# Kernel optimization log

Hardware: AMD Instinct MI355X
Metric: run time of the kernel (lower is better)

Reference implementation:

```python
import jax, jax.numpy as jnp
import numpy as np


def _next_pow2(n: int) -> int:
    return 1 << (int(n) - 1).bit_length()


def setup_inputs() -> dict:
    key = jax.random.key(0)
    k1, k2 = jax.random.split(key)
    B, T, L = 256, 65536, 65536  # batch, seq_len, filter length (L >= T so epoched recurrence == full causal conv)
    x = jax.random.normal(k1, (B, T), dtype=jnp.float32)
    filt = jax.random.normal(k2, (1, L), dtype=jnp.float32) / np.float32(np.sqrt(L))
    return {"x": x, "filt": filt}


def reference(x, filt):
    """EpochedFutureFill.forward == causal FIR convolution of x with filt.

    The torch module's per-token loop (sliced dot-product + FFT-refreshed
    FutureFill cache every K steps) computes exactly
        y[:, t] = sum_{s=0}^{t} filt[0, s] * x[:, t - s]
    for t < T <= L. We express that directly as one FFT convolution,
    mirroring the module's own future_fill (pow-2 rfft/irfft) math.
    """
    B, T = x.shape
    L = filt.shape[-1]
    n_fft = _next_pow2(T + L - 1)
    xf = jnp.fft.rfft(x, n=n_fft)        # (B, n_fft//2+1) complex
    ff = jnp.fft.rfft(filt, n=n_fft)     # (1, n_fft//2+1) complex, broadcasts over batch
    y_full = jnp.fft.irfft(xf * ff, n=n_fft)
    return y_full[:, :T]                 # causal part: (B, T)
```

## Files before the change

kernel.cpp:

```cpp
#include <hip/hip_runtime.h>


#define N_FFT 131072
#define N1    512
#define N2    256
#define T_LEN 65536
#define CB    128
#define PI_F  3.14159265358979323846f
#define R2_F  0.70710678118654752f
#define C16F  0.92387953251128675613f
#define S16F  0.38268343236508977173f

typedef __attribute__((ext_vector_type(2))) __fp16 h2;
typedef __attribute__((ext_vector_type(4))) __fp16 h4;
typedef __attribute__((ext_vector_type(8))) __fp16 h8;

__device__ inline int brev9(int x) { return (int)(__brev((unsigned)x) >> 23); }

__device__ inline float2 cadd(float2 a, float2 b){ return make_float2(a.x+b.x, a.y+b.y); }
__device__ inline float2 csub(float2 a, float2 b){ return make_float2(a.x-b.x, a.y-b.y); }
__device__ inline float2 cmul(float2 a, float2 b){ return make_float2(a.x*b.x-a.y*b.y, a.x*b.y+a.y*b.x); }
__device__ inline float2 cmulc(float2 a, float2 b){ return make_float2(a.x*b.x+a.y*b.y, a.y*b.x-a.x*b.y); }
__device__ inline float2 csq(float2 a){ return make_float2(a.x*a.x-a.y*a.y, 2.f*a.x*a.y); }
__device__ inline float2 conjf(float2 a){ return make_float2(a.x, -a.y); }
__device__ inline float2 expif(float a){ float s,c; __sincosf(a,&s,&c); return make_float2(c,s); }
__device__ inline h2 f2h(float2 v){ return __builtin_amdgcn_cvt_pkrtz(v.x, v.y); }

__device__ inline float2 mul_mi(float2 a){ return make_float2(a.y, -a.x); }
__device__ inline float2 mul_pi(float2 a){ return make_float2(-a.y, a.x); }
__device__ inline float2 mul_w81(float2 a){ return make_float2(R2_F*(a.x+a.y), R2_F*(a.y-a.x)); }
__device__ inline float2 mul_w83(float2 a){ return make_float2(R2_F*(a.y-a.x), -R2_F*(a.x+a.y)); }
__device__ inline float2 mul_w81c(float2 a){ return make_float2(R2_F*(a.x-a.y), R2_F*(a.x+a.y)); }
__device__ inline float2 mul_w83c(float2 a){ return make_float2(-R2_F*(a.x+a.y), R2_F*(a.x-a.y)); }

__device__ __forceinline__ void lgkm_barrier(){
    asm volatile("s_waitcnt lgkmcnt(0)" ::: "memory");
    __builtin_amdgcn_s_barrier();
    __builtin_amdgcn_sched_barrier(0);
}

__device__ inline void dif4(float2&a0, float2&a1, float2&a2, float2&a3, float2 w1, float2 w2){
    float2 s02 = cadd(a0,a2), d02 = csub(a0,a2);
    float2 s13 = cadd(a1,a3), d13 = csub(a1,a3);
    float2 b2 = cmul(w1,d02);
    float2 t  = cmul(w1,d13);
    float2 b3 = make_float2(t.y, -t.x);
    a0 = cadd(s02,s13);
    a1 = cmul(w2, csub(s02,s13));
    a2 = cadd(b2,b3);
    a3 = cmul(w2, csub(b2,b3));
}

__device__ inline void dit4i(float2&a0, float2&a1, float2&a2, float2&a3, float2 w1, float2 w2){
    float2 t1 = cmul(w1,a1), t3 = cmul(w1,a3);
    float2 u0 = cadd(a0,t1), u1 = csub(a0,t1);
    float2 u2 = cadd(a2,t3), u3 = csub(a2,t3);
    float2 s2 = cmul(w2,u2), s3 = cmul(w2,u3);
    a0 = cadd(u0,s2); a2 = csub(u0,s2);
    a1 = make_float2(u1.x - s3.y, u1.y + s3.x);
    a3 = make_float2(u1.x + s3.y, u1.y - s3.x);
}

__device__ constexpr int BR[16] = {0,8,4,12,2,10,6,14,1,9,5,13,3,11,7,15};

__device__ __forceinline__ void fft16_fwd(float2 v[16]){
    {
        float2 s02=cadd(v[0],v[8]),  d02=csub(v[0],v[8]);
        float2 s13=cadd(v[4],v[12]), d13=csub(v[4],v[12]);
        float2 b3 = mul_mi(d13);
        v[0]=cadd(s02,s13); v[4]=csub(s02,s13);
        v[8]=cadd(d02,b3);  v[12]=csub(d02,b3);
    }
    {
        float2 s02=cadd(v[1],v[9]),  d02=csub(v[1],v[9]);
        float2 s13=cadd(v[5],v[13]), d13=csub(v[5],v[13]);
        const float2 w1 = make_float2(C16F,-S16F);
        float2 b2 = cmul(w1,d02), b3 = mul_mi(cmul(w1,d13));
        v[1]=cadd(s02,s13);  v[5]=mul_w81(csub(s02,s13));
        v[9]=cadd(b2,b3);    v[13]=mul_w81(csub(b2,b3));
    }
    {
        float2 s02=cadd(v[2],v[10]), d02=csub(v[2],v[10]);
        float2 s13=cadd(v[6],v[14]), d13=csub(v[6],v[14]);
        float2 b2 = mul_w81(d02), b3 = mul_mi(mul_w81(d13));
        v[2]=cadd(s02,s13);  v[6]=mul_mi(csub(s02,s13));
        v[10]=cadd(b2,b3);   v[14]=mul_mi(csub(b2,b3));
    }
    {
        float2 s02=cadd(v[3],v[11]), d02=csub(v[3],v[11]);
        float2 s13=cadd(v[7],v[15]), d13=csub(v[7],v[15]);
        const float2 w1 = make_float2(S16F,-C16F);
        float2 b2 = cmul(w1,d02), b3 = mul_mi(cmul(w1,d13));
        v[3]=cadd(s02,s13);  v[7]=mul_w83(csub(s02,s13));
        v[11]=cadd(b2,b3);   v[15]=mul_w83(csub(b2,b3));
    }
#pragma unroll
    for (int q=0;q<4;q++){
        float2 a0=v[4*q],a1=v[4*q+1],a2=v[4*q+2],a3=v[4*q+3];
        float2 s02=cadd(a0,a2), d02=csub(a0,a2);
        float2 s13=cadd(a1,a3), d13=csub(a1,a3);
        float2 b3 = mul_mi(d13);
        v[4*q]=cadd(s02,s13);   v[4*q+1]=csub(s02,s13);
        v[4*q+2]=cadd(d02,b3);  v[4*q+3]=csub(d02,b3);
    }
}

__device__ __forceinline__ void fft16_inv(float2 v[16]){
#pragma unroll
    for (int q=0;q<4;q++){
        float2 a0=v[4*q],a1=v[4*q+1],a2=v[4*q+2],a3=v[4*q+3];
        float2 u0=cadd(a0,a1), u1=csub(a0,a1);
        float2 u2=cadd(a2,a3), u3=csub(a2,a3);
        v[4*q]=cadd(u0,u2);   v[4*q+2]=csub(u0,u2);
        v[4*q+1]=make_float2(u1.x-u3.y, u1.y+u3.x);
        v[4*q+3]=make_float2(u1.x+u3.y, u1.y-u3.x);
    }
    {
        float2 t1=v[4], t3=v[12];
        float2 u0=cadd(v[0],t1), u1=csub(v[0],t1);
        float2 u2=cadd(v[8],t3), u3=csub(v[8],t3);
        v[0]=cadd(u0,u2); v[8]=csub(u0,u2);
        v[4]=make_float2(u1.x-u3.y, u1.y+u3.x);
        v[12]=make_float2(u1.x+u3.y, u1.y-u3.x);
    }
    {
        float2 t1=mul_w81c(v[5]), t3=mul_w81c(v[13]);
        float2 u0=cadd(v[1],t1), u1=csub(v[1],t1);
        float2 u2=cadd(v[9],t3), u3=csub(v[9],t3);
        const float2 w2 = make_float2(C16F,S16F);
        float2 s2=cmul(w2,u2), s3=cmul(w2,u3);
        v[1]=cadd(u0,s2); v[9]=csub(u0,s2);
        v[5]=make_float2(u1.x-s3.y, u1.y+s3.x);
        v[13]=make_float2(u1.x+s3.y, u1.y-s3.x);
    }
    {
        float2 t1=mul_pi(v[6]), t3=mul_pi(v[14]);
        float2 u0=cadd(v[2],t1), u1=csub(v[2],t1);
        float2 u2=cadd(v[10],t3), u3=csub(v[10],t3);
        float2 s2=mul_w81c(u2), s3=mul_w81c(u3);
        v[2]=cadd(u0,s2); v[10]=csub(u0,s2);
        v[6]=make_float2(u1.x-s3.y, u1.y+s3.x);
        v[14]=make_float2(u1.x+s3.y, u1.y-s3.x);
    }
    {
        float2 t1=mul_w83c(v[7]), t3=mul_w83c(v[15]);
        float2 u0=cadd(v[3],t1), u1=csub(v[3],t1);
        float2 u2=cadd(v[11],t3), u3=csub(v[11],t3);
        const float2 w2 = make_float2(S16F,C16F);
        float2 s2=cmul(w2,u2), s3=cmul(w2,u3);
        v[3]=cadd(u0,s2); v[11]=csub(u0,s2);
        v[7]=make_float2(u1.x-s3.y, u1.y+s3.x);
        v[15]=make_float2(u1.x+s3.y, u1.y-s3.x);
    }
}

template<bool HALF>
__global__ __launch_bounds__(256, 4) void fwd_cols(
    const float* __restrict__ re_base, const float* __restrict__ im_base,
    long long row_stride, void* __restrict__ dstv)
{
    __shared__ __align__(16) float2 s[16 * 290];
    const int tid = threadIdx.x;
    const int tile = blockIdx.x, row = blockIdx.y;
    const int n2base = tile * 16;
    const int n2l = tid & 15, q = tid >> 4;
    const int n2 = n2base + n2l;

    const float* rp = re_base + (long long)row * row_stride;
    const float* ip = im_base ? (im_base + (long long)row * row_stride) : nullptr;

    float2 vE[16], vO[16];
    if (ip) {
#pragma unroll
        for (int p = 0; p < 16; p++) {
            int g = (16 * p + q) * N2 + n2;
            vE[p] = make_float2(rp[g], ip[g]);
        }
    } else {
#pragma unroll
        for (int p = 0; p < 16; p++) {
            int g = (16 * p + q) * N2 + n2;
            vE[p] = make_float2(rp[g], 0.f);
        }
    }
    {
        constexpr float WC[16] = {
            1.f, 0.98078528040323044913f, 0.92387953251128675613f, 0.83146961230254523708f,
            0.70710678118654752440f, 0.55557023301960222474f, 0.38268343236508977173f,
            0.19509032201612826785f, 0.f, -0.19509032201612826785f, -0.38268343236508977173f,
            -0.55557023301960222474f, -0.70710678118654752440f, -0.83146961230254523708f,
            -0.92387953251128675613f, -0.98078528040323044913f };
        constexpr float WS[16] = {
            0.f, -0.19509032201612826785f, -0.38268343236508977173f, -0.55557023301960222474f,
            -0.70710678118654752440f, -0.83146961230254523708f, -0.92387953251128675613f,
            -0.98078528040323044913f, -1.f, -0.98078528040323044913f, -0.92387953251128675613f,
            -0.83146961230254523708f, -0.70710678118654752440f, -0.55557023301960222474f,
            -0.38268343236508977173f, -0.19509032201612826785f };
        vO[0] = vE[0];
#pragma unroll
        for (int p = 1; p < 16; p++) vO[p] = cmul(vE[p], make_float2(WC[p], WS[p]));
    }
    fft16_fwd(vE);
    fft16_fwd(vO);

    const float2 u = expif((float)q * (-2.f * PI_F / 512.f));
    float2 w = make_float2(1.f, 0.f);
    const int exbase = n2l * 290;
    const float thN = -2.f * PI_F / (float)N_FFT;
    const float2 stpN = expif(thN * (float)(32 * n2));

#pragma unroll
    for (int h = 0; h < 2; h++) {
#pragma unroll
        for (int t = 0; t < 8; t++) {
            int tt = t + 8 * h;
            int rl = 2 * t;
            s[exbase + rl * 18 + q]       = cmul(vE[BR[tt]], w);  w = cmul(w, u);
            s[exbase + (rl + 1) * 18 + q] = cmul(vO[BR[tt]], w);  w = cmul(w, u);
        }
        lgkm_barrier();

        float2 b[16];
        {
            const float4* z4 = (const float4*)(s + exbase + q * 18);
#pragma unroll
            for (int j = 0; j < 8; j++) {
                float4 A = z4[j];
                b[2*j]   = make_float2(A.x, A.y);
                b[2*j+1] = make_float2(A.z, A.w);
            }
        }
        fft16_fwd(b);

        const int rpr = 16 * h + q;
        float2 wb = expif(thN * (float)(n2 * rpr));
#pragma unroll
        for (int m = 0; m < 16; m++) {
            float2 rv = cmul(b[BR[m]], wb);
            int k1 = rpr + 32 * m;
            if (HALF) {
                h2* drow = (h2*)dstv + (size_t)row * N_FFT;
                drow[(size_t)k1 * N2 + n2] = f2h(rv);
            } else {
                float2* drow = (float2*)dstv + (size_t)row * N_FFT;
                drow[(size_t)k1 * N2 + n2] = rv;
            }
            if (m < 15) wb = cmul(wb, stpN);
        }
        if (h == 0) lgkm_barrier();
    }
}

#define RPITCH 18

__global__ __launch_bounds__(128) void fwd_rows_g(float2* __restrict__ G)
{
    __shared__ __align__(16) float2 s[8 * 16 * RPITCH + 16 * RPITCH];
    const int tid = threadIdx.x;
    const int t = tid & 15, rl = tid >> 4;
    const long long row = (long long)blockIdx.x * 8 + rl;
    float2* tab = s + 8 * 16 * RPITCH;

    {
        int b0 = tid >> 4, c0 = tid & 15;
        tab[b0 * RPITCH + c0] = expif((float)(b0 * c0) * (-2.f * PI_F / 256.f));
        int e = tid + 128, b1 = e >> 4, c1 = e & 15;
        tab[b1 * RPITCH + c1] = expif((float)(b1 * c1) * (-2.f * PI_F / 256.f));
    }
    __syncthreads();

    const float2* gp = G + (size_t)row * N2 + t;
    float2 v[16];
#pragma unroll
    for (int a = 0; a < 16; a++) v[a] = gp[16 * a];

    fft16_fwd(v);
#pragma unroll
    for (int p = 1; p < 16; p++) v[p] = cmul(v[p], tab[t * RPITCH + BR[p]]);

    float2* rS = s + rl * (16 * RPITCH);
    float4* rS4 = (float4*)rS;
#pragma unroll
    for (int k = 0; k < 8; k++) {
        float2 e = v[BR[2*k]], o = v[BR[2*k] + 8];
        rS4[(t * RPITCH + 2*k) >> 1] = make_float4(e.x, e.y, o.x, o.y);
    }
    asm volatile("s_waitcnt lgkmcnt(0)" ::: "memory");
#pragma unroll
    for (int b = 0; b < 16; b++) v[b] = rS[b * RPITCH + t];

    fft16_fwd(v);

    float4* o4 = (float4*)(G + (size_t)row * N2 + 16 * t);
#pragma unroll
    for (int m = 0; m < 8; m++)
        o4[m] = make_float4(v[2*m].x, v[2*m].y, v[2*m+1].x, v[2*m+1].y);
}

__global__ __launch_bounds__(256, 4) void mid_rows(
    h2* __restrict__ buf, const float2* __restrict__ Gh)
{
    __shared__ __align__(16) float2 s[16 * 16 * RPITCH + 16 * RPITCH];
    const int tid = threadIdx.x;
    const int t = tid & 15, rl = tid >> 4;
    const long long row = (long long)blockIdx.x * 16 + rl;
    const int k1 = (int)(row & (N1 - 1));
    float2* tab = s + 16 * 16 * RPITCH;

    {
        int b = tid >> 4, c = tid & 15;
        tab[b * RPITCH + c] = expif((float)(b * c) * (-2.f * PI_F / 256.f));
    }
    __syncthreads();

    h2* bp = buf + ((size_t)row * N2 + t);
    float2 v[16];
#pragma unroll
    for (int a = 0; a < 16; a++) {
        h2 h = bp[16 * a];
        v[a] = make_float2((float)h.x, (float)h.y);
    }

    fft16_fwd(v);
#pragma unroll
    for (int p = 1; p < 16; p++) v[p] = cmul(v[p], tab[t * RPITCH + BR[p]]);

    float2* rS = s + rl * (16 * RPITCH);
    float4* rS4 = (float4*)rS;
#pragma unroll
    for (int k = 0; k < 8; k++) {
        float2 e = v[BR[2*k]], o = v[BR[2*k] + 8];
        rS4[(t * RPITCH + 2*k) >> 1] = make_float4(e.x, e.y, o.x, o.y);
    }

    const float4* g4 = (const float4*)(Gh + ((size_t)k1 * N2 + 16 * t));
    float4 g[8];
#pragma unroll
    for (int m = 0; m < 8; m++) g[m] = g4[m];

    asm volatile("s_waitcnt lgkmcnt(0)" ::: "memory");
#pragma unroll
    for (int b = 0; b < 16; b++) v[b] = rS[b * RPITCH + t];

    fft16_fwd(v);

#pragma unroll
    for (int m = 0; m < 8; m++) {
        v[2*m]   = cmul(v[2*m],   make_float2(g[m].x, g[m].y));
        v[2*m+1] = cmul(v[2*m+1], make_float2(g[m].z, g[m].w));
    }

    fft16_inv(v);
#pragma unroll
    for (int b = 1; b < 16; b++) v[b] = cmulc(v[b], tab[b * RPITCH + t]);

#pragma unroll
    for (int m = 0; m < 8; m++)
        rS4[(t * RPITCH + 2*m) >> 1] = make_float4(v[2*m].x, v[2*m].y, v[2*m+1].x, v[2*m+1].y);
    asm volatile("s_waitcnt lgkmcnt(0)" ::: "memory");
#pragma unroll
    for (int c = 0; c < 16; c++) v[BR[c]] = rS[c * RPITCH + t];

    fft16_inv(v);

    {
        const float th = 2.f * PI_F / (float)N_FFT;
        float2 w = expif((float)(k1 * t) * th);
        const float2 stp = expif((float)(16 * k1) * th);
#pragma unroll
        for (int a = 0; a < 16; a++) {
            float2 r = cmul(v[a], w);
            bp[16 * a] = f2h(r);
            if (a < 15) w = cmul(w, stp);
        }
    }
}

__global__ __launch_bounds__(512, 4) void inv_cols(
    const h2* __restrict__ src, float* __restrict__ out)
{
    __shared__ float4 s4[N1 * 16 / 2];
    float2* s = (float2*)s4;
    const int tile = blockIdx.x, row = blockIdx.y, tid = threadIdx.x;
    const int n2base = tile * 16;
    const h2* srow = src + (size_t)row * N_FFT;
    const int cp = tid & 7, r8 = tid >> 3;

#pragma unroll
    for (int i = 0; i < 8; i++) {
        int k1 = r8 + 64 * i;
        h4 v = *((const h4*)(srow + (size_t)k1 * N2 + n2base + 2 * cp));
        int p = brev9(k1);
        s4[p * 8 + cp] = make_float4((float)v.x, (float)v.y, (float)v.z, (float)v.w);
    }
    __syncthreads();

    const int c = tid & 15, r = tid >> 4;

    const float2 w1c = make_float2(0.f, 1.f);
    const float2 w2c = make_float2(R2_F, R2_F);
    const float2 one = make_float2(1.f, 0.f);
#pragma unroll
    for (int o = 0; o < 2; o++) {
        int base = 8 * (r + 32 * o);
        float2 v[8];
#pragma unroll
        for (int m = 0; m < 8; m++) v[m] = s[(base + m) * 16 + c];
#pragma unroll
        for (int m = 0; m < 8; m += 2) {
            float2 a = v[m], b = v[m + 1];
            v[m] = cadd(a, b); v[m + 1] = csub(a, b);
        }
        dit4i(v[0], v[2], v[4], v[6], one, one);
        dit4i(v[1], v[3], v[5], v[7], w1c, w2c);
#pragma unroll
        for (int m = 0; m < 8; m++) s[(base + m) * 16 + c] = v[m];
    }
    __syncthreads();

    {
        float2 w2 = expif((float)(r & 7) * (PI_F / 16.f));
        float2 w1 = csq(w2);
#pragma unroll
        for (int qq = 0; qq < 4; qq++) {
            int g = (r >> 3) + 4 * qq;
            int p0 = g * 32 + (r & 7);
            float2 a0 = s[p0*16+c], a1 = s[(p0+8)*16+c], a2 = s[(p0+16)*16+c], a3 = s[(p0+24)*16+c];
            dit4i(a0, a1, a2, a3, w1, w2);
            s[p0*16+c] = a0; s[(p0+8)*16+c] = a1; s[(p0+16)*16+c] = a2; s[(p0+24)*16+c] = a3;
        }
    }
    __syncthreads();
    {
        float2 w2 = expif((float)r * (PI_F / 64.f));
        float2 w1 = csq(w2);
#pragma unroll
        for (int qq = 0; qq < 4; qq++) {
            int p0 = qq * 128 + r;
            float2 a0 = s[p0*16+c], a1 = s[(p0+32)*16+c], a2 = s[(p0+64)*16+c], a3 = s[(p0+96)*16+c];
            dit4i(a0, a1, a2, a3, w1, w2);
            s[p0*16+c] = a0; s[(p0+32)*16+c] = a1; s[(p0+64)*16+c] = a2; s[(p0+96)*16+c] = a3;
        }
    }
    __syncthreads();
    {
        float2 w2 = expif((float)r * (PI_F / 256.f));
        const float2 stp = make_float2(0.92387953251f, 0.38268343236f);
#pragma unroll
        for (int qq = 0; qq < 4; qq++) {
            int j = r + 32 * qq;
            float2 w1 = csq(w2);
            float2 a0 = s[j*16+c], a1 = s[(j+128)*16+c], a2 = s[(j+256)*16+c], a3 = s[(j+384)*16+c];
            dit4i(a0, a1, a2, a3, w1, w2);
            s[j*16+c] = a0; s[(j+128)*16+c] = a1; s[(j+256)*16+c] = a2; s[(j+384)*16+c] = a3;
            w2 = cmul(w2, stp);
        }
    }
    __syncthreads();

    const float scale = 1.0f / (float)N_FFT;
    float* out0 = out + (size_t)(2 * row) * T_LEN;
    float* out1 = out + (size_t)(2 * row + 1) * T_LEN;
#pragma unroll
    for (int i = 0; i < 4; i++) {
        int p = r8 + 64 * i;
        float4 q = s4[p * 8 + cp];
        int n = p * N2 + n2base + 2 * cp;
        *(float2*)(out0 + n) = make_float2(q.x * scale, q.z * scale);
        *(float2*)(out1 + n) = make_float2(q.y * scale, q.w * scale);
    }
}

extern "C" void kernel_launch(void* const* d_in, const int* in_sizes, int n_in,
                              void* d_out, int out_size, void* d_ws, size_t ws_size,
                              hipStream_t stream) {
    const float* x    = (const float*)d_in[0];
    const float* filt = (const float*)d_in[1];
    float* out = (float*)d_out;

    h2* buf = (h2*)d_ws;
    float2* G = (float2*)((char*)d_ws + (size_t)CB * N_FFT * sizeof(h2));

    fwd_cols<false><<<dim3(16, 1), 256, 0, stream>>>(filt, nullptr, 0LL, (void*)G);
    fwd_rows_g<<<N1 / 8, 128, 0, stream>>>(G);
    fwd_cols<true><<<dim3(16, CB), 256, 0, stream>>>(x, x + T_LEN, (long long)(2 * T_LEN), (void*)buf);
    mid_rows<<<(CB * N1) / 16, 256, 0, stream>>>(buf, G);
    inv_cols<<<dim3(16, CB), 512, 0, stream>>>(buf, out);
}
```

Baseline: 224.2 us.

## Restructure inverse column FFT as register radix-16 passes with one LDS exchange

Rewrites inv_cols so each thread loads 32 column samples directly into registers and runs two register-resident 16-point inverse FFTs with twiddles. A single padded LDS transpose then feeds a second pair of 16-point FFTs and a final radix-2 combine. This replaces the earlier sequence of radix-2/4 stages, each separated by a block barrier and a full LDS round trip. The block shrinks from 512 to 256 threads with more registers per thread, which may lower occupancy. Global loads become 4-byte h2 reads instead of 8-byte h4, and output stores become scalar writes instead of float2.

After: 221.0 us. No clear change (-1.4%).

```diff
diff --git a/kernel.cpp b/kernel.cpp
--- a/kernel.cpp
+++ b/kernel.cpp
@@ -37,28 +37,6 @@
     asm volatile("s_waitcnt lgkmcnt(0)" ::: "memory");
     __builtin_amdgcn_s_barrier();
     __builtin_amdgcn_sched_barrier(0);
-}
-
-__device__ inline void dif4(float2&a0, float2&a1, float2&a2, float2&a3, float2 w1, float2 w2){
-    float2 s02 = cadd(a0,a2), d02 = csub(a0,a2);
-    float2 s13 = cadd(a1,a3), d13 = csub(a1,a3);
-    float2 b2 = cmul(w1,d02);
-    float2 t  = cmul(w1,d13);
-    float2 b3 = make_float2(t.y, -t.x);
-    a0 = cadd(s02,s13);
-    a1 = cmul(w2, csub(s02,s13));
-    a2 = cadd(b2,b3);
-    a3 = cmul(w2, csub(b2,b3));
-}
-
-__device__ inline void dit4i(float2&a0, float2&a1, float2&a2, float2&a3, float2 w1, float2 w2){
-    float2 t1 = cmul(w1,a1), t3 = cmul(w1,a3);
-    float2 u0 = cadd(a0,t1), u1 = csub(a0,t1);
-    float2 u2 = cadd(a2,t3), u3 = csub(a2,t3);
-    float2 s2 = cmul(w2,u2), s3 = cmul(w2,u3);
-    a0 = cadd(u0,s2); a2 = csub(u0,s2);
-    a1 = make_float2(u1.x - s3.y, u1.y + s3.x);
-    a3 = make_float2(u1.x + s3.y, u1.y - s3.x);
 }
 
 __device__ constexpr int BR[16] = {0,8,4,12,2,10,6,14,1,9,5,13,3,11,7,15};
@@ -376,98 +354,102 @@
     }
 }
 
-__global__ __launch_bounds__(512, 4) void inv_cols(
+__global__ __launch_bounds__(256, 4) void inv_cols(
     const h2* __restrict__ src, float* __restrict__ out)
 {
-    __shared__ float4 s4[N1 * 16 / 2];
-    float2* s = (float2*)s4;
-    const int tile = blockIdx.x, row = blockIdx.y, tid = threadIdx.x;
+    __shared__ __align__(16) float2 s[16 * 290];
+    const int tid = threadIdx.x;
+    const int tile = blockIdx.x, row = blockIdx.y;
     const int n2base = tile * 16;
+    const int n2l = tid & 15, u = tid >> 4;
+    const int n2 = n2base + n2l;
     const h2* srow = src + (size_t)row * N_FFT;
-    const int cp = tid & 7, r8 = tid >> 3;
-
-#pragma unroll
-    for (int i = 0; i < 8; i++) {
-        int k1 = r8 + 64 * i;
-        h4 v = *((const h4*)(srow + (size_t)k1 * N2 + n2base + 2 * cp));
-        int p = brev9(k1);
-        s4[p * 8 + cp] = make_float4((float)v.x, (float)v.y, (float)v.z, (float)v.w);
-    }
-    __syncthreads();
-
-    const int c = tid & 15, r = tid >> 4;
-
-    const float2 w1c = make_float2(0.f, 1.f);
-    const float2 w2c = make_float2(R2_F, R2_F);
-    const float2 one = make_float2(1.f, 0.f);
-#pragma unroll
-    for (int o = 0; o < 2; o++) {
-        int base = 8 * (r + 32 * o);
-        float2 v[8];
-#pragma unroll
-        for (int m = 0; m < 8; m++) v[m] = s[(base + m) * 16 + c];
-#pragma unroll
-        for (int m = 0; m < 8; m += 2) {
-            float2 a = v[m], b = v[m + 1];
-            v[m] = cadd(a, b); v[m + 1] = csub(a, b);
-        }
-        dit4i(v[0], v[2], v[4], v[6], one, one);
-        dit4i(v[1], v[3], v[5], v[7], w1c, w2c);
-#pragma unroll
-        for (int m = 0; m < 8; m++) s[(base + m) * 16 + c] = v[m];
-    }
-    __syncthreads();
-
-    {
-        float2 w2 = expif((float)(r & 7) * (PI_F / 16.f));
-        float2 w1 = csq(w2);
-#pragma unroll
-        for (int qq = 0; qq < 4; qq++) {
-            int g = (r >> 3) + 4 * qq;
-            int p0 = g * 32 + (r & 7);
-            float2 a0 = s[p0*16+c], a1 = s[(p0+8)*16+c], a2 = s[(p0+16)*16+c], a3 = s[(p0+24)*16+c];
-            dit4i(a0, a1, a2, a3, w1, w2);
-            s[p0*16+c] = a0; s[(p0+8)*16+c] = a1; s[(p0+16)*16+c] = a2; s[(p0+24)*16+c] = a3;
-        }
-    }
-    __syncthreads();
-    {
-        float2 w2 = expif((float)r * (PI_F / 64.f));
-        float2 w1 = csq(w2);
-#pragma unroll
-        for (int qq = 0; qq < 4; qq++) {
-            int p0 = qq * 128 + r;
-            float2 a0 = s[p0*16+c], a1 = s[(p0+32)*16+c], a2 = s[(p0+64)*16+c], a3 = s[(p0+96)*16+c];
-            dit4i(a0, a1, a2, a3, w1, w2);
-            s[p0*16+c] = a0; s[(p0+32)*16+c] = a1; s[(p0+64)*16+c] = a2; s[(p0+96)*16+c] = a3;
-        }
-    }
-    __syncthreads();
-    {
-        float2 w2 = expif((float)r * (PI_F / 256.f));
-        const float2 stp = make_float2(0.92387953251f, 0.38268343236f);
-#pragma unroll
-        for (int qq = 0; qq < 4; qq++) {
-            int j = r + 32 * qq;
-            float2 w1 = csq(w2);
-            float2 a0 = s[j*16+c], a1 = s[(j+128)*16+c], a2 = s[(j+256)*16+c], a3 = s[(j+384)*16+c];
-            dit4i(a0, a1, a2, a3, w1, w2);
-            s[j*16+c] = a0; s[(j+128)*16+c] = a1; s[(j+256)*16+c] = a2; s[(j+384)*16+c] = a3;
-            w2 = cmul(w2, stp);
-        }
-    }
-    __syncthreads();
-
-    const float scale = 1.0f / (float)N_FFT;
-    float* out0 = out + (size_t)(2 * row) * T_LEN;
-    float* out1 = out + (size_t)(2 * row + 1) * T_LEN;
-#pragma unroll
-    for (int i = 0; i < 4; i++) {
-        int p = r8 + 64 * i;
-        float4 q = s4[p * 8 + cp];
-        int n = p * N2 + n2base + 2 * cp;
-        *(float2*)(out0 + n) = make_float2(q.x * scale, q.z * scale);
-        *(float2*)(out1 + n) = make_float2(q.y * scale, q.w * scale);
+
+    float2 vA[16], vB[16];
+#pragma unroll
+    for (int ss = 0; ss < 16; ss++) {
+        h2 a = srow[(size_t)(u + 32 * ss) * N2 + n2];
+        vA[BR[ss]] = make_float2((float)a.x, (float)a.y);
+    }
+#pragma unroll
+    for (int ss = 0; ss < 16; ss++) {
+        h2 a = srow[(size_t)(u + 16 + 32 * ss) * N2 + n2];
+        vB[BR[ss]] = make_float2((float)a.x, (float)a.y);
+    }
+    fft16_inv(vA);
+    fft16_inv(vB);
+
+    {
+        const float2 e1 = expif((float)u        * (2.f * PI_F / 512.f));
+        const float2 e2 = expif((float)(u + 16) * (2.f * PI_F / 512.f));
+        float2 w1 = e1, w2 = e2;
+#pragma unroll
+        for (int qq = 1; qq < 16; qq++) {
+            vA[qq] = cmul(vA[qq], w1);
+            vB[qq] = cmul(vB[qq], w2);
+            if (qq < 15) { w1 = cmul(w1, e1); w2 = cmul(w2, e2); }
+        }
+    }
+
+    const int exb = n2l * 290;
+    float2 bE[16], bO[16];
+
+#pragma unroll
+    for (int qq = 0; qq < 16; qq++)
+        s[exb + qq * 18 + u] = vA[qq];
+    lgkm_barrier();
+    {
+        const float4* z4 = (const float4*)(s + exb + u * 18);
+#pragma unroll
+        for (int j = 0; j < 8; j++) {
+            float4 A = z4[j];
+            bE[BR[j]] = make_float2(A.x, A.y);
+            bO[BR[j]] = make_float2(A.z, A.w);
+        }
+    }
+    lgkm_barrier();
+
+#pragma unroll
+    for (int qq = 0; qq < 16; qq++)
+        s[exb + qq * 18 + u] = vB[qq];
+    lgkm_barrier();
+    {
+        const float4* z4 = (const float4*)(s + exb + u * 18);
+#pragma unroll
+        for (int j = 0; j < 8; j++) {
+            float4 A = z4[j];
+            bE[BR[8 + j]] = make_float2(A.x, A.y);
+            bO[BR[8 + j]] = make_float2(A.z, A.w);
+        }
+    }
+
+    fft16_inv(bE);
+    fft16_inv(bO);
+
+    {
+        constexpr float WCI[16] = {
+            1.f, 0.98078528040323044913f, 0.92387953251128675613f, 0.83146961230254523708f,
+            0.70710678118654752440f, 0.55557023301960222474f, 0.38268343236508977173f,
+            0.19509032201612826785f, 0.f, -0.19509032201612826785f, -0.38268343236508977173f,
+            -0.55557023301960222474f, -0.70710678118654752440f, -0.83146961230254523708f,
+            -0.92387953251128675613f, -0.98078528040323044913f };
+        constexpr float WSI[16] = {
+            0.f, 0.19509032201612826785f, 0.38268343236508977173f, 0.55557023301960222474f,
+            0.70710678118654752440f, 0.83146961230254523708f, 0.92387953251128675613f,
+            0.98078528040323044913f, 1.f, 0.98078528040323044913f, 0.92387953251128675613f,
+            0.83146961230254523708f, 0.70710678118654752440f, 0.55557023301960222474f,
+            0.38268343236508977173f, 0.19509032201612826785f };
+        const float scale = 1.0f / (float)N_FFT;
+        float* out0 = out + (size_t)(2 * row) * T_LEN;
+        float* out1 = out + (size_t)(2 * row + 1) * T_LEN;
+#pragma unroll
+        for (int p = 0; p < 16; p++) {
+            float2 o = (p == 0) ? bO[0] : cmul(bO[p], make_float2(WCI[p], WSI[p]));
+            float2 y = cadd(bE[p], o);
+            int n = (16 * p + u) * N2 + n2;
+            out0[n] = y.x * scale;
+            out1[n] = y.y * scale;
+        }
     }
 }
 
@@ -485,5 +467,5 @@
     fwd_rows_g<<<N1 / 8, 128, 0, stream>>>(G);
     fwd_cols<true><<<dim3(16, CB), 256, 0, stream>>>(x, x + T_LEN, (long long)(2 * T_LEN), (void*)buf);
     mid_rows<<<(CB * N1) / 16, 256, 0, stream>>>(buf, G);
-    inv_cols<<<dim3(16, CB), 512, 0, stream>>>(buf, out);
-}
+    inv_cols<<<dim3(16, CB), 256, 0, stream>>>(buf, out);
+}
```
